# Optimization experiments

Measured on AMD Instinct MI355X. Metric: run time of the kernel, lower is better.

## Reference

```python
import jax, jax.numpy as jnp
import numpy as np

N_NODES = 2_000_000
IN_CH = 64
OUT_CH = 128
NUM_GRAPHS = 16384


def setup_inputs() -> dict:
    key = jax.random.key(0)
    k1, k2, k3, k4 = jax.random.split(key, 4)
    x = jax.random.normal(k1, (N_NODES, IN_CH), dtype=jnp.float32)
    segment_ids = jnp.sort(
        jax.random.randint(k2, (N_NODES,), 0, NUM_GRAPHS, dtype=jnp.int64)
    )
    # nn.Linear(in, out): weight [out, in], bias [out]
    bound = 1.0 / np.sqrt(IN_CH)
    weight = jax.random.uniform(k3, (OUT_CH, IN_CH), dtype=jnp.float32,
                                minval=-bound, maxval=bound)
    bias = jax.random.uniform(k4, (OUT_CH,), dtype=jnp.float32,
                              minval=-bound, maxval=bound)
    return {"x": x, "segment_ids": segment_ids, "weight": weight,
            "bias": bias, "num_graphs": NUM_GRAPHS}


def reference(x, segment_ids, weight, bias, num_graphs):
    # Per-graph mean pooling (segment mean), then linear embed.
    sums = jax.ops.segment_sum(x, segment_ids, num_segments=num_graphs)  # [G, d]
    counts = jax.ops.segment_sum(jnp.ones((x.shape[0],), x.dtype),
                                 segment_ids, num_segments=num_graphs)  # [G]
    means = sums / counts[:, None]                                       # [G, d]
    return means @ weight.T + bias                                        # [G, out]
```

## Files before the change

kernel.cpp:

```cpp
#include <hip/hip_runtime.h>
#include <hip/hip_bf16.h>


#define IN_CH 64
#define OUT_CH 128
#define RPW 256
#define ABLK 256
#define BBLK 512
#define BGRID 512

typedef float f32x4 __attribute__((ext_vector_type(4)));

__device__ __forceinline__ void flush_seg(float* __restrict__ sums,
                                          int* __restrict__ counts,
                                          int g, int l, int cq,
                                          f32x4& acc, int& ccnt) {
    float ax = acc.x, ay = acc.y, az = acc.z, aw = acc.w;
    ax += __shfl_xor(ax, 16); ay += __shfl_xor(ay, 16);
    az += __shfl_xor(az, 16); aw += __shfl_xor(aw, 16);
    ax += __shfl_xor(ax, 32); ay += __shfl_xor(ay, 32);
    az += __shfl_xor(az, 32); aw += __shfl_xor(aw, 32);
    int tot = ccnt;
    tot += __shfl_xor(tot, 16);
    tot += __shfl_xor(tot, 32);
    if (l < 16) {
        float* p = sums + (size_t)g * IN_CH + cq;
        atomicAdd(p + 0, ax);
        atomicAdd(p + 1, ay);
        atomicAdd(p + 2, az);
        atomicAdd(p + 3, aw);
    }
    if (l == 0) atomicAdd(counts + g, tot);
    acc.x = 0.f; acc.y = 0.f; acc.z = 0.f; acc.w = 0.f;
    ccnt = 0;
}

__global__ __launch_bounds__(ABLK) void seg_accum_kernel(
        const float* __restrict__ x, const int* __restrict__ ids,
        float* __restrict__ sums, int* __restrict__ counts, int N) {
    const int t = threadIdx.x;
    const int w = blockIdx.x * (ABLK / 64) + (t >> 6);
    const int l = t & 63;
    const int row0 = w * RPW;
    if (row0 >= N) return;
    int row_end = row0 + RPW;
    if (row_end > N) row_end = N;

    const int rs = l >> 4;
    const int cq = (l & 15) << 2;

    f32x4 acc; acc.x = 0.f; acc.y = 0.f; acc.z = 0.f; acc.w = 0.f;
    int ccnt = 0;
    int cur_g = ids[row0];

    for (int r = row0; r < row_end; r += 4) {
        const int id = ids[r + rs];
        const f32x4 v = __builtin_nontemporal_load(
            reinterpret_cast<const f32x4*>(x + (size_t)(r + rs) * IN_CH + cq));
        if (__all(id == cur_g)) {
            acc.x += v.x; acc.y += v.y; acc.z += v.z; acc.w += v.w;
            ++ccnt;
        } else {
            #pragma unroll
            for (int k = 0; k < 4; ++k) {
                const int gk = __shfl(id, k * 16);
                if (gk != cur_g) {
                    flush_seg(sums, counts, cur_g, l, cq, acc, ccnt);
                    cur_g = gk;
                }
                if (rs == k) {
                    acc.x += v.x; acc.y += v.y; acc.z += v.z; acc.w += v.w;
                    ++ccnt;
                }
            }
        }
    }
    flush_seg(sums, counts, cur_g, l, cq, acc, ccnt);
}

__global__ __launch_bounds__(BBLK) void mean_linear_kernel(
        const float* __restrict__ sums, const int* __restrict__ counts,
        const float* __restrict__ W, const float* __restrict__ bias,
        float* __restrict__ out, int G) {
    __shared__ float w_lds[IN_CH * 129];
    const int t = threadIdx.x;
    for (int i = t; i < OUT_CH * IN_CH; i += BBLK) {
        const int o = i >> 6, c = i & 63;
        w_lds[c * 129 + o] = W[i];
    }
    __syncthreads();

    const int wv = t >> 6, l = t & 63;
    const int cq = (l & 15) << 2;
    const float b0 = bias[l], b1 = bias[l + 64];

    for (int g = blockIdx.x * (BBLK / 64) + wv; g < G; g += BGRID * (BBLK / 64)) {
        const float cnt = (float)counts[g];
        const f32x4 s = *reinterpret_cast<const f32x4*>(
            sums + (size_t)g * IN_CH + cq);
        const float m0 = s.x / cnt, m1 = s.y / cnt;
        const float m2 = s.z / cnt, m3 = s.w / cnt;

        float o0 = b0, o1 = b1;
        #pragma unroll
        for (int c = 0; c < IN_CH; ++c) {
            float m;
            switch (c & 3) {
                case 0:  m = __shfl(m0, c >> 2); break;
                case 1:  m = __shfl(m1, c >> 2); break;
                case 2:  m = __shfl(m2, c >> 2); break;
                default: m = __shfl(m3, c >> 2); break;
            }
            o0 = fmaf(w_lds[c * 129 + l],      m, o0);
            o1 = fmaf(w_lds[c * 129 + l + 64], m, o1);
        }
        out[(size_t)g * OUT_CH + l]      = o0;
        out[(size_t)g * OUT_CH + l + 64] = o1;
    }
}

#define WPB 8
#define BLOCK (WPB * 64)
__global__ __launch_bounds__(BLOCK) void fused_pool_linear_kernel(
        const float* __restrict__ x, const int* __restrict__ ids,
        const float* __restrict__ W, const float* __restrict__ bias,
        float* __restrict__ out, int N, int G) {
    __shared__ float w_lds[IN_CH * 129];
    const int t  = threadIdx.x;
    const int wv = t >> 6;
    const int l  = t & 63;
    const int g  = blockIdx.x * WPB + wv;

    int s0 = 0, s1 = 0;
    if (g < G) {
        const int target = g + (l & 1);
        int lo = 0, hi = N;
        const int guess = (int)(((long long)target * (long long)N) / (long long)G);
        int wlo = guess - 4096; if (wlo < 0) wlo = 0;
        int whi = guess + 4096; if (whi > N) whi = N;
        const bool ok_lo = (wlo == 0) || (ids[wlo - 1] < target);
        const bool ok_hi = (whi == N) || (ids[whi] >= target);
        if (ok_lo && ok_hi) { lo = wlo; hi = whi; }
        while (lo < hi) {
            const int mid = (lo + hi) >> 1;
            if (ids[mid] < target) lo = mid + 1; else hi = mid;
        }
        s0 = __shfl(lo, 0);
        s1 = __shfl(lo, 1);
    }
    for (int i = t; i < OUT_CH * IN_CH; i += BLOCK) {
        const int o = i >> 6, c = i & 63;
        w_lds[c * 129 + o] = W[i];
    }
    __syncthreads();
    if (g >= G) return;

    const int rs = l >> 4;
    const int cq = (l & 15) << 2;
    float4 a0 = make_float4(0.f, 0.f, 0.f, 0.f);
    float4 a1 = make_float4(0.f, 0.f, 0.f, 0.f);
    int r = s0;
    for (; r + 8 <= s1; r += 8) {
        const f32x4 v0 = __builtin_nontemporal_load(
            reinterpret_cast<const f32x4*>(x + (size_t)(r + rs) * IN_CH + cq));
        const f32x4 v1 = __builtin_nontemporal_load(
            reinterpret_cast<const f32x4*>(x + (size_t)(r + 4 + rs) * IN_CH + cq));
        a0.x += v0.x; a0.y += v0.y; a0.z += v0.z; a0.w += v0.w;
        a1.x += v1.x; a1.y += v1.y; a1.z += v1.z; a1.w += v1.w;
    }
    if (r + 4 <= s1) {
        const f32x4 v = __builtin_nontemporal_load(
            reinterpret_cast<const f32x4*>(x + (size_t)(r + rs) * IN_CH + cq));
        a0.x += v.x; a0.y += v.y; a0.z += v.z; a0.w += v.w;
        r += 4;
    }
    if (r + rs < s1) {
        const f32x4 v = __builtin_nontemporal_load(
            reinterpret_cast<const f32x4*>(x + (size_t)(r + rs) * IN_CH + cq));
        a1.x += v.x; a1.y += v.y; a1.z += v.z; a1.w += v.w;
    }
    float sx = a0.x + a1.x, sy = a0.y + a1.y;
    float sz = a0.z + a1.z, sw = a0.w + a1.w;
    sx += __shfl_xor(sx, 16); sy += __shfl_xor(sy, 16);
    sz += __shfl_xor(sz, 16); sw += __shfl_xor(sw, 16);
    sx += __shfl_xor(sx, 32); sy += __shfl_xor(sy, 32);
    sz += __shfl_xor(sz, 32); sw += __shfl_xor(sw, 32);
    const float cnt = (float)(s1 - s0);
    const float m0 = sx / cnt, m1 = sy / cnt, m2 = sz / cnt, m3 = sw / cnt;
    float o0 = bias[l], o1 = bias[l + 64];
    #pragma unroll
    for (int c = 0; c < IN_CH; ++c) {
        float m;
        switch (c & 3) {
            case 0:  m = __shfl(m0, c >> 2); break;
            case 1:  m = __shfl(m1, c >> 2); break;
            case 2:  m = __shfl(m2, c >> 2); break;
            default: m = __shfl(m3, c >> 2); break;
        }
        o0 = fmaf(w_lds[c * 129 + l],      m, o0);
        o1 = fmaf(w_lds[c * 129 + l + 64], m, o1);
    }
    out[(size_t)g * OUT_CH + l]      = o0;
    out[(size_t)g * OUT_CH + l + 64] = o1;
}

extern "C" void kernel_launch(void* const* d_in, const int* in_sizes, int n_in,
                              void* d_out, int out_size, void* d_ws, size_t ws_size,
                              hipStream_t stream) {
    const float* x    = (const float*)d_in[0];
    const int*   ids  = (const int*)d_in[1];
    const float* W    = (const float*)d_in[2];
    const float* bias = (const float*)d_in[3];
    float* out = (float*)d_out;

    const int N = in_sizes[1];
    const int G = out_size / OUT_CH;

    const size_t sums_bytes = (size_t)G * IN_CH * sizeof(float);
    const size_t need = sums_bytes + (size_t)G * sizeof(int);

    if (ws_size >= need) {
        float* sums   = (float*)d_ws;
        int*   counts = (int*)((char*)d_ws + sums_bytes);
        hipMemsetAsync(d_ws, 0, need, stream);
        const int waves   = (N + RPW - 1) / RPW;
        const int ablocks = (waves + (ABLK / 64) - 1) / (ABLK / 64);
        seg_accum_kernel<<<ablocks, ABLK, 0, stream>>>(x, ids, sums, counts, N);
        mean_linear_kernel<<<BGRID, BBLK, 0, stream>>>(sums, counts, W, bias, out, G);
    } else {
        const int blocks = (G + WPB - 1) / WPB;
        fused_pool_linear_kernel<<<blocks, BLOCK, 0, stream>>>(
            x, ids, W, bias, out, N, G);
    }
}
```

Baseline: 124.4 us.

## Precompute segment boundaries via ballot and stream runs without per-row id checks

The segment-accumulate kernel now loads all 256 segment ids of a wave's chunk up front, finds boundaries with a shuffle-up compare and ballot masks, then streams each contiguous run with an unrolled two-accumulator loop before one atomic flush. This removes the per-iteration id load, the __all vote and the divergent per-row flush path from the main loop, so loads can be issued back to back. The per-run tail handling adds some overhead when segments are short relative to the chunk, and the streaming loop is shared with the fallback fused kernel.

```diff
diff --git a/kernel.cpp b/kernel.cpp
--- a/kernel.cpp
+++ b/kernel.cpp
@@ -6,33 +6,54 @@
 #define OUT_CH 128
 #define RPW 256
 #define ABLK 256
-#define BBLK 512
-#define BGRID 512
+#define LBLK 512
+#define LGRID 512
 
 typedef float f32x4 __attribute__((ext_vector_type(4)));
 
-__device__ __forceinline__ void flush_seg(float* __restrict__ sums,
+__device__ __forceinline__ f32x4 ntload(const float* p) {
+    return __builtin_nontemporal_load(reinterpret_cast<const f32x4*>(p));
+}
+
+__device__ __forceinline__ void stream_seg(const float* __restrict__ x,
+                                           int s0, int s1, int rs, int cq,
+                                           float& sx, float& sy,
+                                           float& sz, float& sw) {
+    f32x4 a0 = {0.f, 0.f, 0.f, 0.f};
+    f32x4 a1 = {0.f, 0.f, 0.f, 0.f};
+    int r = s0;
+    for (; r + 8 <= s1; r += 8) {
+        const f32x4 v0 = ntload(x + (size_t)(r + rs)     * IN_CH + cq);
+        const f32x4 v1 = ntload(x + (size_t)(r + 4 + rs) * IN_CH + cq);
+        a0 += v0; a1 += v1;
+    }
+    if (r + 4 <= s1) {
+        a0 += ntload(x + (size_t)(r + rs) * IN_CH + cq);
+        r += 4;
+    }
+    if (r + rs < s1) {
+        a1 += ntload(x + (size_t)(r + rs) * IN_CH + cq);
+    }
+    const f32x4 a = a0 + a1;
+    sx = a.x; sy = a.y; sz = a.z; sw = a.w;
+    sx += __shfl_xor(sx, 16); sy += __shfl_xor(sy, 16);
+    sz += __shfl_xor(sz, 16); sw += __shfl_xor(sw, 16);
+    sx += __shfl_xor(sx, 32); sy += __shfl_xor(sy, 32);
+    sz += __shfl_xor(sz, 32); sw += __shfl_xor(sw, 32);
+}
+
+__device__ __forceinline__ void flush_run(float* __restrict__ sums,
                                           int* __restrict__ counts,
-                                          int g, int l, int cq,
-                                          f32x4& acc, int& ccnt) {
-    float ax = acc.x, ay = acc.y, az = acc.z, aw = acc.w;
-    ax += __shfl_xor(ax, 16); ay += __shfl_xor(ay, 16);
-    az += __shfl_xor(az, 16); aw += __shfl_xor(aw, 16);
-    ax += __shfl_xor(ax, 32); ay += __shfl_xor(ay, 32);
-    az += __shfl_xor(az, 32); aw += __shfl_xor(aw, 32);
-    int tot = ccnt;
-    tot += __shfl_xor(tot, 16);
-    tot += __shfl_xor(tot, 32);
+                                          int g, int l, int cq, int len,
+                                          float sx, float sy, float sz, float sw) {
     if (l < 16) {
         float* p = sums + (size_t)g * IN_CH + cq;
-        atomicAdd(p + 0, ax);
-        atomicAdd(p + 1, ay);
-        atomicAdd(p + 2, az);
-        atomicAdd(p + 3, aw);
-    }
-    if (l == 0) atomicAdd(counts + g, tot);
-    acc.x = 0.f; acc.y = 0.f; acc.z = 0.f; acc.w = 0.f;
-    ccnt = 0;
+        atomicAdd(p + 0, sx);
+        atomicAdd(p + 1, sy);
+        atomicAdd(p + 2, sz);
+        atomicAdd(p + 3, sw);
+    }
+    if (l == 0) atomicAdd(counts + g, len);
 }
 
 __global__ __launch_bounds__(ABLK) void seg_accum_kernel(
@@ -43,48 +64,55 @@
     const int l = t & 63;
     const int row0 = w * RPW;
     if (row0 >= N) return;
-    int row_end = row0 + RPW;
-    if (row_end > N) row_end = N;
+    const int row_end = (row0 + RPW < N) ? row0 + RPW : N;
 
     const int rs = l >> 4;
     const int cq = (l & 15) << 2;
 
-    f32x4 acc; acc.x = 0.f; acc.y = 0.f; acc.z = 0.f; acc.w = 0.f;
-    int ccnt = 0;
-    int cur_g = ids[row0];
-
-    for (int r = row0; r < row_end; r += 4) {
-        const int id = ids[r + rs];
-        const f32x4 v = __builtin_nontemporal_load(
-            reinterpret_cast<const f32x4*>(x + (size_t)(r + rs) * IN_CH + cq));
-        if (__all(id == cur_g)) {
-            acc.x += v.x; acc.y += v.y; acc.z += v.z; acc.w += v.w;
-            ++ccnt;
-        } else {
-            #pragma unroll
-            for (int k = 0; k < 4; ++k) {
-                const int gk = __shfl(id, k * 16);
-                if (gk != cur_g) {
-                    flush_seg(sums, counts, cur_g, l, cq, acc, ccnt);
-                    cur_g = gk;
-                }
-                if (rs == k) {
-                    acc.x += v.x; acc.y += v.y; acc.z += v.z; acc.w += v.w;
-                    ++ccnt;
-                }
-            }
-        }
-    }
-    flush_seg(sums, counts, cur_g, l, cq, acc, ccnt);
-}
-
-__global__ __launch_bounds__(BBLK) void mean_linear_kernel(
+    int idv[4];
+    #pragma unroll
+    for (int k = 0; k < 4; ++k) {
+        const int p = row0 + 64 * k + l;
+        idv[k] = ids[p < N ? p : (N - 1)];
+    }
+
+    unsigned long long tm[4];
+    #pragma unroll
+    for (int k = 0; k < 4; ++k) {
+        int prev = __shfl_up(idv[k], 1);
+        if (k > 0 && l == 0) prev = __shfl(idv[k - 1], 63);
+        const int p = row0 + 64 * k + l;
+        const bool tr = (p > row0) && (p < row_end) && (idv[k] != prev);
+        tm[k] = __ballot(tr);
+    }
+
+    int run_start = row0;
+    int g = __shfl(idv[0], 0);
+    float sx, sy, sz, sw;
+    #pragma unroll
+    for (int k = 0; k < 4; ++k) {
+        unsigned long long m = tm[k];
+        while (m) {
+            const int b = __builtin_ctzll(m);
+            m &= m - 1;
+            const int pos = row0 + 64 * k + b;
+            stream_seg(x, run_start, pos, rs, cq, sx, sy, sz, sw);
+            flush_run(sums, counts, g, l, cq, pos - run_start, sx, sy, sz, sw);
+            run_start = pos;
+            g = __shfl(idv[k], b);
+        }
+    }
+    stream_seg(x, run_start, row_end, rs, cq, sx, sy, sz, sw);
+    flush_run(sums, counts, g, l, cq, row_end - run_start, sx, sy, sz, sw);
+}
+
+__global__ __launch_bounds__(LBLK) void mean_linear_kernel(
         const float* __restrict__ sums, const int* __restrict__ counts,
         const float* __restrict__ W, const float* __restrict__ bias,
         float* __restrict__ out, int G) {
     __shared__ float w_lds[IN_CH * 129];
     const int t = threadIdx.x;
-    for (int i = t; i < OUT_CH * IN_CH; i += BBLK) {
+    for (int i = t; i < OUT_CH * IN_CH; i += LBLK) {
         const int o = i >> 6, c = i & 63;
         w_lds[c * 129 + o] = W[i];
     }
@@ -94,7 +122,7 @@
     const int cq = (l & 15) << 2;
     const float b0 = bias[l], b1 = bias[l + 64];
 
-    for (int g = blockIdx.x * (BBLK / 64) + wv; g < G; g += BGRID * (BBLK / 64)) {
+    for (int g = blockIdx.x * (LBLK / 64) + wv; g < G; g += LGRID * (LBLK / 64)) {
         const float cnt = (float)counts[g];
         const f32x4 s = *reinterpret_cast<const f32x4*>(
             sums + (size_t)g * IN_CH + cq);
@@ -157,34 +185,8 @@
 
     const int rs = l >> 4;
     const int cq = (l & 15) << 2;
-    float4 a0 = make_float4(0.f, 0.f, 0.f, 0.f);
-    float4 a1 = make_float4(0.f, 0.f, 0.f, 0.f);
-    int r = s0;
-    for (; r + 8 <= s1; r += 8) {
-        const f32x4 v0 = __builtin_nontemporal_load(
-            reinterpret_cast<const f32x4*>(x + (size_t)(r + rs) * IN_CH + cq));
-        const f32x4 v1 = __builtin_nontemporal_load(
-            reinterpret_cast<const f32x4*>(x + (size_t)(r + 4 + rs) * IN_CH + cq));
-        a0.x += v0.x; a0.y += v0.y; a0.z += v0.z; a0.w += v0.w;
-        a1.x += v1.x; a1.y += v1.y; a1.z += v1.z; a1.w += v1.w;
-    }
-    if (r + 4 <= s1) {
-        const f32x4 v = __builtin_nontemporal_load(
-            reinterpret_cast<const f32x4*>(x + (size_t)(r + rs) * IN_CH + cq));
-        a0.x += v.x; a0.y += v.y; a0.z += v.z; a0.w += v.w;
-        r += 4;
-    }
-    if (r + rs < s1) {
-        const f32x4 v = __builtin_nontemporal_load(
-            reinterpret_cast<const f32x4*>(x + (size_t)(r + rs) * IN_CH + cq));
-        a1.x += v.x; a1.y += v.y; a1.z += v.z; a1.w += v.w;
-    }
-    float sx = a0.x + a1.x, sy = a0.y + a1.y;
-    float sz = a0.z + a1.z, sw = a0.w + a1.w;
-    sx += __shfl_xor(sx, 16); sy += __shfl_xor(sy, 16);
-    sz += __shfl_xor(sz, 16); sw += __shfl_xor(sw, 16);
-    sx += __shfl_xor(sx, 32); sy += __shfl_xor(sy, 32);
-    sz += __shfl_xor(sz, 32); sw += __shfl_xor(sw, 32);
+    float sx, sy, sz, sw;
+    stream_seg(x, s0, s1, rs, cq, sx, sy, sz, sw);
     const float cnt = (float)(s1 - s0);
     const float m0 = sx / cnt, m1 = sy / cnt, m2 = sz / cnt, m3 = sw / cnt;
     float o0 = bias[l], o1 = bias[l + 64];
@@ -226,7 +228,7 @@
         const int waves   = (N + RPW - 1) / RPW;
         const int ablocks = (waves + (ABLK / 64) - 1) / (ABLK / 64);
         seg_accum_kernel<<<ablocks, ABLK, 0, stream>>>(x, ids, sums, counts, N);
-        mean_linear_kernel<<<BGRID, BBLK, 0, stream>>>(sums, counts, W, bias, out, G);
+        mean_linear_kernel<<<LGRID, LBLK, 0, stream>>>(sums, counts, W, bias, out, G);
     } else {
         const int blocks = (G + WPB - 1) / WPB;
         fused_pool_linear_kernel<<<blocks, BLOCK, 0, stream>>>(
```

After: 133.7 us. 7.5% more time.
